# Performance work log

Measured on AMD Instinct MI355X. Metric: run time of the kernel, lower is better.

Reference implementation:

```python
import jax, jax.numpy as jnp
import numpy as np

# geomloss SamplesLoss('sinkhorn', p=2, blur=0.05, scaling=0.5, debias=True) math
P = 2
BLUR = 0.05
SCALING = 0.5
DIAMETER = 64.0  # static conservative bound on point-cloud diameter for randn D=64 data


def _eps_schedule():
    eps_list = []
    e = DIAMETER ** P
    target = BLUR ** P
    while e > target:
        eps_list.append(e)
        e *= SCALING ** P
    eps_list.append(target)
    return np.array(eps_list, dtype=np.float32)


def _cost(x, y):
    # C_ij = ||x_i - y_j||^2 / 2   (p=2 cost of geomloss)
    sq = (jnp.sum(x * x, -1)[:, :, None] * 0.5
          + jnp.sum(y * y, -1)[:, None, :] * 0.5
          - jnp.einsum('bnd,bmd->bnm', x, y))
    return jnp.maximum(sq, 0.0)


def _softmin(eps, C, h):
    # f_i = -eps * log sum_j exp(h_j - C_ij / eps);  C: (B,N,M), h: (B,M)
    return -eps * jax.nn.logsumexp(h[:, None, :] - C / eps, axis=-1)


def setup_inputs() -> dict:
    key = jax.random.key(0)
    k1, k2, k3, k4 = jax.random.split(key, 4)
    B, N, M, D = 8, 2048, 2048, 64
    x = jax.random.normal(k1, (B, N, D), dtype=jnp.float32)
    y = jax.random.normal(k2, (B, M, D), dtype=jnp.float32)
    w1 = jax.random.uniform(k3, (B, N), dtype=jnp.float32) + 0.01
    w2 = jax.random.uniform(k4, (B, M), dtype=jnp.float32) + 0.01
    w1 = w1 / jnp.sum(w1, axis=-1, keepdims=True)
    w2 = w2 / jnp.sum(w2, axis=-1, keepdims=True)
    return {'x': x, 'y': y, 'w1': w1, 'w2': w2}


def _sinkhorn_divergence(x, y, w1, w2):
    a_log = jnp.log(w1)
    b_log = jnp.log(w2)
    eps_list = jnp.asarray(_eps_schedule())

    # --- Sinkhorn loop on detached quantities (geomloss detaches the loop) ---
    xd = jax.lax.stop_gradient(x)
    yd = jax.lax.stop_gradient(y)
    ald = jax.lax.stop_gradient(a_log)
    bld = jax.lax.stop_gradient(b_log)
    C_xy_d = _cost(xd, yd)
    C_yx_d = jnp.swapaxes(C_xy_d, 1, 2)
    C_xx_d = _cost(xd, xd)
    C_yy_d = _cost(yd, yd)

    eps0 = eps_list[0]
    f_ab = _softmin(eps0, C_xy_d, bld)
    g_ba = _softmin(eps0, C_yx_d, ald)
    f_aa = _softmin(eps0, C_xx_d, ald)
    g_bb = _softmin(eps0, C_yy_d, bld)

    def step(carry, eps):
        f_ab, g_ba, f_aa, g_bb = carry
        ft = _softmin(eps, C_xy_d, bld + g_ba / eps)
        gt = _softmin(eps, C_yx_d, ald + f_ab / eps)
        f_aa_t = _softmin(eps, C_xx_d, ald + f_aa / eps)
        g_bb_t = _softmin(eps, C_yy_d, bld + g_bb / eps)
        return (0.5 * (f_ab + ft), 0.5 * (g_ba + gt),
                0.5 * (f_aa + f_aa_t), 0.5 * (g_bb + g_bb_t)), None

    (f_ab, g_ba, f_aa, g_bb), _ = jax.lax.scan(step, (f_ab, g_ba, f_aa, g_bb), eps_list)

    # --- last extrapolation at eps = blur^p, differentiable ---
    eps = eps_list[-1]
    C_xy = _cost(x, y)
    C_yx = jnp.swapaxes(C_xy, 1, 2)
    C_xx = _cost(x, x)
    C_yy = _cost(y, y)
    f_ab_f = _softmin(eps, C_xy, b_log + g_ba / eps)
    g_ba_f = _softmin(eps, C_yx, a_log + f_ab / eps)
    f_aa_f = _softmin(eps, C_xx, a_log + f_aa / eps)
    g_bb_f = _softmin(eps, C_yy, b_log + g_bb / eps)

    # debiased sinkhorn cost per batch element
    loss = (jnp.sum(w1 * (f_ab_f - f_aa_f), axis=-1)
            + jnp.sum(w2 * (g_ba_f - g_bb_f), axis=-1))
    return loss


def reference(x, y, w1, w2):
    loss = _sinkhorn_divergence(x, y, w1, w2)
    return jnp.mean(loss)  # reduction='mean'
```

## Files before the change

kernel.cpp:

```cpp
#include <hip/hip_runtime.h>

#define NB 8
#define NN 2048
#define MM 2048
#define DD 64
#define NCHK 16
#define TS 128
#define L2E 1.4426950408889634f
#define LN2 0.6931471805599453f

typedef _Float16 half_t;
typedef __attribute__((ext_vector_type(8))) _Float16 f16x8;
typedef __attribute__((ext_vector_type(4))) float f32x4;

__device__ half_t g_xh[NB * NN * DD];
__device__ half_t g_yh[NB * MM * DD];
__device__ float g_fab[3][NB * NN], g_gba[3][NB * NN];
__device__ float g_faa[3][NB * NN], g_gbb[3][NB * NN];
__device__ float g_alog[NB * NN], g_blog[NB * NN];
__device__ float g_xn[NB * NN], g_yn[NB * NN];
__device__ float g_h0[NB * MM], g_h1[NB * NN], g_h2[NB * NN], g_h3[NB * MM];
__device__ float2 g_pfab[NB * NCHK * NN];
__device__ float2 g_pgba[NB * NCHK * NN];
__device__ float2 g_pfaa[NB * NCHK * NN];
__device__ float2 g_pgbb[NB * NCHK * NN];

__global__ __launch_bounds__(256) void prep_kernel(
    const float* __restrict__ x, const float* __restrict__ y,
    const float* __restrict__ w1, const float* __restrict__ w2)
{
  int gid = blockIdx.x * 256 + threadIdx.x;
  if (gid < NB * NN) {
    g_alog[gid] = log2f(w1[gid]);
    g_blog[gid] = log2f(w2[gid]);
  }
  int lane = threadIdx.x & 63;
  int row = blockIdx.x * 4 + (threadIdx.x >> 6);
  float xv = x[(size_t)row * DD + lane];
  float yv = y[(size_t)row * DD + lane];
  g_xh[(size_t)row * DD + lane] = (half_t)xv;
  g_yh[(size_t)row * DD + lane] = (half_t)yv;
  float sx = xv * xv;
  float sy = yv * yv;
#pragma unroll
  for (int off = 32; off > 0; off >>= 1) {
    sx += __shfl_down(sx, off);
    sy += __shfl_down(sy, off);
  }
  if (lane == 0) {
    g_xn[row] = 0.5f * sx;
    g_yn[row] = 0.5f * sy;
  }
}

__global__ __launch_bounds__(256) void hprep_kernel(
    const float* __restrict__ fab_in, const float* __restrict__ gba_in,
    const float* __restrict__ faa_in, const float* __restrict__ gbb_in,
    float gs2)
{
  int i = blockIdx.x * 256 + threadIdx.x;
  g_h0[i] = fmaf(gs2, gba_in[i], g_blog[i]);
  g_h1[i] = fmaf(gs2, fab_in[i], g_alog[i]);
  g_h2[i] = fmaf(gs2, faa_in[i], g_alog[i]);
  g_h3[i] = fmaf(gs2, gbb_in[i], g_blog[i]);
}

struct FusedArgs {
  const half_t* Af;
  const half_t* Bf;
  const float* nrow;
  const float* ncol;
  const float* hrow;
  const float* hcol;
  float2* prow;
  float2* pcol;
  int sym;
};

union SharedU {
  half_t stage[2][TS * DD];
  struct {
    float redR[TS][17], redC[TS][17];
    float rowM[TS], colM[TS];
  } r;
};

__global__ __launch_bounds__(256) void tile_fused(
    FusedArgs T0, FusedArgs T1, FusedArgs T2, float keps)
{
  int u = blockIdx.x;
  int slab, b, I, J;
  if (u < 2048) {
    slab = 0; b = u >> 8;
    int tt = u & 255; I = tt >> 4; J = tt & 15;
  } else {
    int v = u - 2048;
    slab = 1 + v / 1088;
    int w2 = v % 1088;
    b = w2 / 136;
    int rem = w2 % 136, ii = 0;
    while (rem >= NCHK - ii) { rem -= NCHK - ii; ++ii; }
    I = ii; J = ii + rem;
  }
  FusedArgs A = (slab == 0) ? T0 : (slab == 1) ? T1 : T2;

  const int t = threadIdx.x;
  const int w = t >> 6, lane = t & 63;
  const int m = lane & 15, quad = lane >> 4;
  const int i0 = I * TS, j0 = J * TS;

  __shared__ SharedU sh;
  char* lb = (char*)&sh;

  {
    const char* gA = (const char*)(A.Af + ((size_t)b * NN + i0) * DD);
    const char* gB = (const char*)(A.Bf + ((size_t)b * MM + j0) * DD);
#pragma unroll
    for (int k = 0; k < 8; ++k) {
      int seg = w * 8 + k;
      int p = (seg * 1024 + lane * 16) & 16383;
      int row = p >> 7, colb = p & 127;
      int colx = colb ^ ((row & 7) << 4);
      const char* src = (seg < 16 ? gA : gB) + (size_t)row * 128 + colx;
      __builtin_amdgcn_global_load_lds(
          (const __attribute__((address_space(1))) unsigned int*)src,
          (__attribute__((address_space(3))) unsigned int*)(lb + seg * 1024),
          16, 0, 0);
    }
  }

  float4 xr[2], hq[2];
#pragma unroll
  for (int g = 0; g < 2; ++g) {
    size_t ro = (size_t)b * NN + i0 + 32 * w + 16 * g + 4 * quad;
    xr[g] = *(const float4*)(A.nrow + ro);
    hq[g] = *(const float4*)(A.hcol + ro);
  }
  float ynk[8], hr[8];
#pragma unroll
  for (int c = 0; c < 8; ++c) {
    size_t co = (size_t)b * MM + j0 + 16 * c + m;
    ynk[c] = -A.ncol[co] * keps;
    hr[c] = A.hrow[co];
  }
  float xnk[2][4], hcv[2][4];
#pragma unroll
  for (int g = 0; g < 2; ++g) {
    xnk[g][0] = -xr[g].x * keps; xnk[g][1] = -xr[g].y * keps;
    xnk[g][2] = -xr[g].z * keps; xnk[g][3] = -xr[g].w * keps;
    hcv[g][0] = hq[g].x; hcv[g][1] = hq[g].y;
    hcv[g][2] = hq[g].z; hcv[g][3] = hq[g].w;
  }

  __syncthreads();

  f32x4 acc[2][8];
#pragma unroll
  for (int g = 0; g < 2; ++g)
#pragma unroll
    for (int c = 0; c < 8; ++c) acc[g][c] = (f32x4){0.f, 0.f, 0.f, 0.f};

#pragma unroll
  for (int s = 0; s < 2; ++s) {
    int qb = quad * 16 + s * 64;
    int ra0 = 32 * w + m, ra1 = 32 * w + 16 + m;
    f16x8 a0 = *(const f16x8*)(lb + ra0 * 128 + (qb ^ ((ra0 & 7) << 4)));
    f16x8 a1 = *(const f16x8*)(lb + ra1 * 128 + (qb ^ ((ra1 & 7) << 4)));
#pragma unroll
    for (int c = 0; c < 8; ++c) {
      int rb = 16 * c + m;
      f16x8 bf = *(const f16x8*)(lb + 16384 + rb * 128 + (qb ^ ((rb & 7) << 4)));
      acc[0][c] = __builtin_amdgcn_mfma_f32_16x16x32_f16(a0, bf, acc[0][c], 0, 0, 0);
      acc[1][c] = __builtin_amdgcn_mfma_f32_16x16x32_f16(a1, bf, acc[1][c], 0, 0, 0);
    }
  }

  float rm[2][4], cm[8];
#pragma unroll
  for (int g = 0; g < 2; ++g)
#pragma unroll
    for (int r = 0; r < 4; ++r) rm[g][r] = -3.0e38f;
#pragma unroll
  for (int c = 0; c < 8; ++c) cm[c] = -3.0e38f;

#pragma unroll
  for (int g = 0; g < 2; ++g)
#pragma unroll
    for (int c = 0; c < 8; ++c) {
      f32x4 v = acc[g][c];
#pragma unroll
      for (int r = 0; r < 4; ++r) {
        float bse = fminf(fmaf(v[r], keps, xnk[g][r]) + ynk[c], 0.f);
        v[r] = bse;
        rm[g][r] = fmaxf(rm[g][r], bse + hr[c]);
        cm[c] = fmaxf(cm[c], bse + hcv[g][r]);
      }
      acc[g][c] = v;
    }

  __syncthreads();

#pragma unroll
  for (int g = 0; g < 2; ++g)
#pragma unroll
    for (int r = 0; r < 4; ++r)
      sh.r.redR[32 * w + 16 * g + 4 * quad + r][m] = rm[g][r];
#pragma unroll
  for (int c = 0; c < 8; ++c)
    sh.r.redC[16 * c + m][4 * w + quad] = cm[c];
  __syncthreads();
  if (t < TS) {
    float mx = sh.r.redR[t][0];
#pragma unroll
    for (int k = 1; k < 16; ++k) mx = fmaxf(mx, sh.r.redR[t][k]);
    sh.r.rowM[t] = mx;
  } else {
    int tt = t - TS;
    float mx = sh.r.redC[tt][0];
#pragma unroll
    for (int k = 1; k < 16; ++k) mx = fmaxf(mx, sh.r.redC[tt][k]);
    sh.r.colM[tt] = mx;
  }
  __syncthreads();

  float rmv[2][4], cmv[8];
#pragma unroll
  for (int g = 0; g < 2; ++g) {
    float4 q = *(const float4*)&sh.r.rowM[32 * w + 16 * g + 4 * quad];
    rmv[g][0] = q.x; rmv[g][1] = q.y; rmv[g][2] = q.z; rmv[g][3] = q.w;
  }
#pragma unroll
  for (int c = 0; c < 8; ++c) cmv[c] = sh.r.colM[16 * c + m];

  float rs[2][4], cs[8];
#pragma unroll
  for (int g = 0; g < 2; ++g)
#pragma unroll
    for (int r = 0; r < 4; ++r) rs[g][r] = 0.f;
#pragma unroll
  for (int c = 0; c < 8; ++c) cs[c] = 0.f;

#pragma unroll
  for (int g = 0; g < 2; ++g)
#pragma unroll
    for (int c = 0; c < 8; ++c) {
      f32x4 v = acc[g][c];
#pragma unroll
      for (int r = 0; r < 4; ++r) {
        rs[g][r] += __builtin_amdgcn_exp2f(v[r] + hr[c] - rmv[g][r]);
        cs[c] += __builtin_amdgcn_exp2f(v[r] + hcv[g][r] - cmv[c]);
      }
    }

#pragma unroll
  for (int g = 0; g < 2; ++g)
#pragma unroll
    for (int r = 0; r < 4; ++r)
      sh.r.redR[32 * w + 16 * g + 4 * quad + r][m] = rs[g][r];
#pragma unroll
  for (int c = 0; c < 8; ++c)
    sh.r.redC[16 * c + m][4 * w + quad] = cs[c];
  __syncthreads();
  if (t < TS) {
    float s = 0.f;
#pragma unroll
    for (int k = 0; k < 16; ++k) s += sh.r.redR[t][k];
    A.prow[((size_t)b * NCHK + J) * NN + i0 + t] = make_float2(sh.r.rowM[t], s);
  } else {
    int tt = t - TS;
    if (!(A.sym && I == J)) {
      float s = 0.f;
#pragma unroll
      for (int k = 0; k < 16; ++k) s += sh.r.redC[tt][k];
      A.pcol[((size_t)b * NCHK + I) * NN + j0 + tt] = make_float2(sh.r.colM[tt], s);
    }
  }
}

struct MergeArgs {
  const float2* part;
  const float* fold;
  float* fout;
  const float* hbase;
  float* hout;
};

__global__ __launch_bounds__(256) void merge4(
    MergeArgs M0, MergeArgs M1, MergeArgs M2, MergeArgs M3,
    float eps, float alpha, float beta, float nextgs)
{
  MergeArgs A = (blockIdx.z == 0) ? M0 : (blockIdx.z == 1) ? M1
              : (blockIdx.z == 2) ? M2 : M3;
  const int b = blockIdx.y;
  const int i = blockIdx.x * 256 + threadIdx.x;
  float2 p[NCHK];
#pragma unroll
  for (int k = 0; k < NCHK; ++k)
    p[k] = A.part[((size_t)b * NCHK + k) * NN + i];
  float M = p[0].x;
#pragma unroll
  for (int k = 1; k < NCHK; ++k) M = fmaxf(M, p[k].x);
  float S = 0.f;
#pragma unroll
  for (int k = 0; k < NCHK; ++k) S += p[k].y * __builtin_amdgcn_exp2f(p[k].x - M);
  float ft = (-LN2 * eps) * (M + __log2f(S));
  int idx = b * NN + i;
  float fnew = alpha * A.fold[idx] + beta * ft;
  A.fout[idx] = fnew;
  A.hout[idx] = fmaf(nextgs * L2E, fnew, A.hbase[idx]);
}

__global__ __launch_bounds__(256) void loss_kernel(
    const float* __restrict__ w1, const float* __restrict__ w2,
    float* __restrict__ out)
{
  __shared__ float red[256];
  float acc = 0.f;
  for (int idx = threadIdx.x; idx < NB * NN; idx += 256) {
    acc += w1[idx] * (g_fab[2][idx] - g_faa[2][idx])
         + w2[idx] * (g_gba[2][idx] - g_gbb[2][idx]);
  }
  red[threadIdx.x] = acc;
  __syncthreads();
  for (int s = 128; s > 0; s >>= 1) {
    if (threadIdx.x < s) red[threadIdx.x] += red[threadIdx.x + s];
    __syncthreads();
  }
  if (threadIdx.x == 0) out[0] = red[0] * (1.0f / NB);
}

extern "C" void kernel_launch(void* const* d_in, const int* in_sizes, int n_in,
                              void* d_out, int out_size, void* d_ws, size_t ws_size,
                              hipStream_t stream)
{
  const float* x = (const float*)d_in[0];
  const float* y = (const float*)d_in[1];
  const float* w1 = (const float*)d_in[2];
  const float* w2 = (const float*)d_in[3];
  float* out = (float*)d_out;

  half_t *xh, *yh;
  float *xn, *yn;
  float *h0, *h1, *h2, *h3, *fabp, *gbap, *faap, *gbbp, *alog, *blog;
  float2 *pfab, *pgba, *pfaa, *pgbb;
  hipGetSymbolAddress((void**)&xh, HIP_SYMBOL(g_xh));
  hipGetSymbolAddress((void**)&yh, HIP_SYMBOL(g_yh));
  hipGetSymbolAddress((void**)&xn, HIP_SYMBOL(g_xn));
  hipGetSymbolAddress((void**)&yn, HIP_SYMBOL(g_yn));
  hipGetSymbolAddress((void**)&h0, HIP_SYMBOL(g_h0));
  hipGetSymbolAddress((void**)&h1, HIP_SYMBOL(g_h1));
  hipGetSymbolAddress((void**)&h2, HIP_SYMBOL(g_h2));
  hipGetSymbolAddress((void**)&h3, HIP_SYMBOL(g_h3));
  hipGetSymbolAddress((void**)&fabp, HIP_SYMBOL(g_fab));
  hipGetSymbolAddress((void**)&gbap, HIP_SYMBOL(g_gba));
  hipGetSymbolAddress((void**)&faap, HIP_SYMBOL(g_faa));
  hipGetSymbolAddress((void**)&gbbp, HIP_SYMBOL(g_gbb));
  hipGetSymbolAddress((void**)&alog, HIP_SYMBOL(g_alog));
  hipGetSymbolAddress((void**)&blog, HIP_SYMBOL(g_blog));
  hipGetSymbolAddress((void**)&pfab, HIP_SYMBOL(g_pfab));
  hipGetSymbolAddress((void**)&pgba, HIP_SYMBOL(g_pgba));
  hipGetSymbolAddress((void**)&pfaa, HIP_SYMBOL(g_pfaa));
  hipGetSymbolAddress((void**)&pgbb, HIP_SYMBOL(g_pgbb));

  auto fab = [&](int s) { return fabp + (size_t)s * NB * NN; };
  auto gba = [&](int s) { return gbap + (size_t)s * NB * NN; };
  auto faa = [&](int s) { return faap + (size_t)s * NB * NN; };
  auto gbb = [&](int s) { return gbbp + (size_t)s * NB * NN; };

  float eps_list[32];
  int ne = 0;
  {
    double v = 64.0 * 64.0;
    double tgt = 0.05 * 0.05;
    while (v > tgt) { eps_list[ne++] = (float)v; v *= 0.25; }
    eps_list[ne++] = (float)tgt;
  }

  prep_kernel<<<4096, 256, 0, stream>>>(x, y, w1, w2);

  dim3 tg(4224);
  dim3 mg(NN / 256, NB, 4);

  auto launch_iter = [&](float eps, float alpha, float beta, float nextgs,
                         int in, int outsel) {
    float keps = L2E / eps;
    FusedArgs T0 = {xh, yh, xn, yn, h0, h1, pfab, pgba, 0};
    FusedArgs T1 = {xh, xh, xn, xn, h2, h2, pfaa, pfaa, 1};
    FusedArgs T2 = {yh, yh, yn, yn, h3, h3, pgbb, pgbb, 1};
    tile_fused<<<tg, 256, 0, stream>>>(T0, T1, T2, keps);
    MergeArgs M0 = {pfab, fab(in), fab(outsel), alog, h1};
    MergeArgs M1 = {pgba, gba(in), gba(outsel), blog, h0};
    MergeArgs M2 = {pfaa, faa(in), faa(outsel), alog, h2};
    MergeArgs M3 = {pgbb, gbb(in), gbb(outsel), blog, h3};
    merge4<<<mg, 256, 0, stream>>>(M0, M1, M2, M3, eps, alpha, beta, nextgs);
  };

  hprep_kernel<<<64, 256, 0, stream>>>(fab(0), gba(0), faa(0), gbb(0), 0.f);
  launch_iter(eps_list[0], 0.f, 1.f, 1.0f / eps_list[0], 0, 0);

  int cur = 0;
  for (int k = 0; k < ne; ++k) {
    int nxt = 1 - cur;
    float nextgs = 1.0f / ((k < ne - 1) ? eps_list[k + 1] : eps_list[ne - 1]);
    launch_iter(eps_list[k], 0.5f, 0.5f, nextgs, cur, nxt);
    cur = nxt;
  }

  launch_iter(eps_list[ne - 1], 0.f, 1.f, 0.f, cur, 2);

  loss_kernel<<<1, 256, 0, stream>>>(w1, w2, out);
}
```

Baseline: 762.6 us.

## Recompute MFMA tile instead of holding accumulators; use wave shuffles for reductions

The fused tile kernel no longer keeps all 64 accumulator floats live across both passes. It reruns the MFMA products per column block in the sum pass, which lowers register pressure and allows a launch bound of 4 blocks per SM. Row max and sum reductions now use in-wave shuffles. Column reductions go through a small [128][4] shared array instead of the large padded reduction buffers, which cuts shared memory use and the number of barriers. The cost is doubling the MFMA and LDS B-fragment reads, plus extra shuffle instructions.

```diff
diff --git a/kernel.cpp b/kernel.cpp
--- a/kernel.cpp
+++ b/kernel.cpp
@@ -77,15 +77,7 @@
   int sym;
 };
 
-union SharedU {
-  half_t stage[2][TS * DD];
-  struct {
-    float redR[TS][17], redC[TS][17];
-    float rowM[TS], colM[TS];
-  } r;
-};
-
-__global__ __launch_bounds__(256) void tile_fused(
+__global__ __launch_bounds__(256, 4) void tile_fused(
     FusedArgs T0, FusedArgs T1, FusedArgs T2, float keps)
 {
   int u = blockIdx.x;
@@ -109,8 +101,9 @@
   const int m = lane & 15, quad = lane >> 4;
   const int i0 = I * TS, j0 = J * TS;
 
-  __shared__ SharedU sh;
-  char* lb = (char*)&sh;
+  __shared__ __align__(16) char stage[2 * TS * DD * 2];
+  __shared__ __align__(16) float cmaxw[TS][4];
+  __shared__ __align__(16) float csumw[TS][4];
 
   {
     const char* gA = (const char*)(A.Af + ((size_t)b * NN + i0) * DD);
@@ -124,7 +117,7 @@
       const char* src = (seg < 16 ? gA : gB) + (size_t)row * 128 + colx;
       __builtin_amdgcn_global_load_lds(
           (const __attribute__((address_space(1))) unsigned int*)src,
-          (__attribute__((address_space(3))) unsigned int*)(lb + seg * 1024),
+          (__attribute__((address_space(3))) unsigned int*)(stage + seg * 1024),
           16, 0, 0);
     }
   }
@@ -154,126 +147,148 @@
 
   __syncthreads();
 
-  f32x4 acc[2][8];
+  const int qb0 = quad * 16, qb1 = quad * 16 + 64;
+  const int ra0 = 32 * w + m, ra1 = 32 * w + 16 + m;
+  const int sa0 = (ra0 & 7) << 4, sa1 = (ra1 & 7) << 4;
+  f16x8 a00 = *(const f16x8*)(stage + ra0 * 128 + (qb0 ^ sa0));
+  f16x8 a01 = *(const f16x8*)(stage + ra0 * 128 + (qb1 ^ sa0));
+  f16x8 a10 = *(const f16x8*)(stage + ra1 * 128 + (qb0 ^ sa1));
+  f16x8 a11 = *(const f16x8*)(stage + ra1 * 128 + (qb1 ^ sa1));
+
+  float rm[2][4], cm8[8];
 #pragma unroll
   for (int g = 0; g < 2; ++g)
 #pragma unroll
-    for (int c = 0; c < 8; ++c) acc[g][c] = (f32x4){0.f, 0.f, 0.f, 0.f};
-
-#pragma unroll
-  for (int s = 0; s < 2; ++s) {
-    int qb = quad * 16 + s * 64;
-    int ra0 = 32 * w + m, ra1 = 32 * w + 16 + m;
-    f16x8 a0 = *(const f16x8*)(lb + ra0 * 128 + (qb ^ ((ra0 & 7) << 4)));
-    f16x8 a1 = *(const f16x8*)(lb + ra1 * 128 + (qb ^ ((ra1 & 7) << 4)));
-#pragma unroll
-    for (int c = 0; c < 8; ++c) {
-      int rb = 16 * c + m;
-      f16x8 bf = *(const f16x8*)(lb + 16384 + rb * 128 + (qb ^ ((rb & 7) << 4)));
-      acc[0][c] = __builtin_amdgcn_mfma_f32_16x16x32_f16(a0, bf, acc[0][c], 0, 0, 0);
-      acc[1][c] = __builtin_amdgcn_mfma_f32_16x16x32_f16(a1, bf, acc[1][c], 0, 0, 0);
-    }
-  }
-
-  float rm[2][4], cm[8];
-#pragma unroll
-  for (int g = 0; g < 2; ++g)
-#pragma unroll
     for (int r = 0; r < 4; ++r) rm[g][r] = -3.0e38f;
-#pragma unroll
-  for (int c = 0; c < 8; ++c) cm[c] = -3.0e38f;
-
-#pragma unroll
-  for (int g = 0; g < 2; ++g)
-#pragma unroll
-    for (int c = 0; c < 8; ++c) {
-      f32x4 v = acc[g][c];
+
+#pragma unroll
+  for (int c = 0; c < 8; ++c) {
+    const int rb = 16 * c + m, sw = (rb & 7) << 4;
+    const char* bp = stage + 16384 + rb * 128;
+    f16x8 b0 = *(const f16x8*)(bp + (qb0 ^ sw));
+    f16x8 b1 = *(const f16x8*)(bp + (qb1 ^ sw));
+    f32x4 acc0 = {0.f, 0.f, 0.f, 0.f}, acc1 = {0.f, 0.f, 0.f, 0.f};
+    acc0 = __builtin_amdgcn_mfma_f32_16x16x32_f16(a00, b0, acc0, 0, 0, 0);
+    acc0 = __builtin_amdgcn_mfma_f32_16x16x32_f16(a01, b1, acc0, 0, 0, 0);
+    acc1 = __builtin_amdgcn_mfma_f32_16x16x32_f16(a10, b0, acc1, 0, 0, 0);
+    acc1 = __builtin_amdgcn_mfma_f32_16x16x32_f16(a11, b1, acc1, 0, 0, 0);
+    float cmc = -3.0e38f;
+#pragma unroll
+    for (int g = 0; g < 2; ++g) {
+      f32x4 v = g ? acc1 : acc0;
 #pragma unroll
       for (int r = 0; r < 4; ++r) {
         float bse = fminf(fmaf(v[r], keps, xnk[g][r]) + ynk[c], 0.f);
-        v[r] = bse;
         rm[g][r] = fmaxf(rm[g][r], bse + hr[c]);
-        cm[c] = fmaxf(cm[c], bse + hcv[g][r]);
-      }
-      acc[g][c] = v;
-    }
-
-  __syncthreads();
-
-#pragma unroll
-  for (int g = 0; g < 2; ++g)
-#pragma unroll
-    for (int r = 0; r < 4; ++r)
-      sh.r.redR[32 * w + 16 * g + 4 * quad + r][m] = rm[g][r];
-#pragma unroll
-  for (int c = 0; c < 8; ++c)
-    sh.r.redC[16 * c + m][4 * w + quad] = cm[c];
-  __syncthreads();
-  if (t < TS) {
-    float mx = sh.r.redR[t][0];
-#pragma unroll
-    for (int k = 1; k < 16; ++k) mx = fmaxf(mx, sh.r.redR[t][k]);
-    sh.r.rowM[t] = mx;
-  } else {
-    int tt = t - TS;
-    float mx = sh.r.redC[tt][0];
-#pragma unroll
-    for (int k = 1; k < 16; ++k) mx = fmaxf(mx, sh.r.redC[tt][k]);
-    sh.r.colM[tt] = mx;
-  }
-  __syncthreads();
-
-  float rmv[2][4], cmv[8];
-#pragma unroll
-  for (int g = 0; g < 2; ++g) {
-    float4 q = *(const float4*)&sh.r.rowM[32 * w + 16 * g + 4 * quad];
-    rmv[g][0] = q.x; rmv[g][1] = q.y; rmv[g][2] = q.z; rmv[g][3] = q.w;
-  }
-#pragma unroll
-  for (int c = 0; c < 8; ++c) cmv[c] = sh.r.colM[16 * c + m];
-
-  float rs[2][4], cs[8];
-#pragma unroll
-  for (int g = 0; g < 2; ++g)
-#pragma unroll
-    for (int r = 0; r < 4; ++r) rs[g][r] = 0.f;
-#pragma unroll
-  for (int c = 0; c < 8; ++c) cs[c] = 0.f;
-
-#pragma unroll
-  for (int g = 0; g < 2; ++g)
-#pragma unroll
-    for (int c = 0; c < 8; ++c) {
-      f32x4 v = acc[g][c];
-#pragma unroll
-      for (int r = 0; r < 4; ++r) {
-        rs[g][r] += __builtin_amdgcn_exp2f(v[r] + hr[c] - rmv[g][r]);
-        cs[c] += __builtin_amdgcn_exp2f(v[r] + hcv[g][r] - cmv[c]);
+        cmc = fmaxf(cmc, bse + hcv[g][r]);
       }
     }
-
+    cm8[c] = cmc;
+  }
+
+  float rmv[2][4];
 #pragma unroll
   for (int g = 0; g < 2; ++g)
 #pragma unroll
-    for (int r = 0; r < 4; ++r)
-      sh.r.redR[32 * w + 16 * g + 4 * quad + r][m] = rs[g][r];
-#pragma unroll
-  for (int c = 0; c < 8; ++c)
-    sh.r.redC[16 * c + m][4 * w + quad] = cs[c];
+    for (int r = 0; r < 4; ++r) {
+      float v = rm[g][r];
+      v = fmaxf(v, __shfl_xor(v, 1));
+      v = fmaxf(v, __shfl_xor(v, 2));
+      v = fmaxf(v, __shfl_xor(v, 4));
+      v = fmaxf(v, __shfl_xor(v, 8));
+      rmv[g][r] = v;
+    }
+
+#pragma unroll
+  for (int c = 0; c < 8; ++c) {
+    float v = cm8[c];
+    v = fmaxf(v, __shfl_xor(v, 16));
+    v = fmaxf(v, __shfl_xor(v, 32));
+    cm8[c] = v;
+  }
+  if (quad == 0) {
+#pragma unroll
+    for (int c = 0; c < 8; ++c) cmaxw[16 * c + m][w] = cm8[c];
+  }
   __syncthreads();
-  if (t < TS) {
-    float s = 0.f;
-#pragma unroll
-    for (int k = 0; k < 16; ++k) s += sh.r.redR[t][k];
-    A.prow[((size_t)b * NCHK + J) * NN + i0 + t] = make_float2(sh.r.rowM[t], s);
-  } else {
-    int tt = t - TS;
-    if (!(A.sym && I == J)) {
-      float s = 0.f;
-#pragma unroll
-      for (int k = 0; k < 16; ++k) s += sh.r.redC[tt][k];
-      A.pcol[((size_t)b * NCHK + I) * NN + j0 + tt] = make_float2(sh.r.colM[tt], s);
+  float cmv[8];
+#pragma unroll
+  for (int c = 0; c < 8; ++c) {
+    float4 q4 = *(const float4*)cmaxw[16 * c + m];
+    cmv[c] = fmaxf(fmaxf(q4.x, q4.y), fmaxf(q4.z, q4.w));
+  }
+
+  float rs[2][4], cs8[8];
+#pragma unroll
+  for (int g = 0; g < 2; ++g)
+#pragma unroll
+    for (int r = 0; r < 4; ++r) rs[g][r] = 0.f;
+
+#pragma unroll
+  for (int c = 0; c < 8; ++c) {
+    const int rb = 16 * c + m, sw = (rb & 7) << 4;
+    const char* bp = stage + 16384 + rb * 128;
+    f16x8 b0 = *(const f16x8*)(bp + (qb0 ^ sw));
+    f16x8 b1 = *(const f16x8*)(bp + (qb1 ^ sw));
+    f32x4 acc0 = {0.f, 0.f, 0.f, 0.f}, acc1 = {0.f, 0.f, 0.f, 0.f};
+    acc0 = __builtin_amdgcn_mfma_f32_16x16x32_f16(a00, b0, acc0, 0, 0, 0);
+    acc0 = __builtin_amdgcn_mfma_f32_16x16x32_f16(a01, b1, acc0, 0, 0, 0);
+    acc1 = __builtin_amdgcn_mfma_f32_16x16x32_f16(a10, b0, acc1, 0, 0, 0);
+    acc1 = __builtin_amdgcn_mfma_f32_16x16x32_f16(a11, b1, acc1, 0, 0, 0);
+    float csc = 0.f;
+#pragma unroll
+    for (int g = 0; g < 2; ++g) {
+      f32x4 v = g ? acc1 : acc0;
+#pragma unroll
+      for (int r = 0; r < 4; ++r) {
+        float bse = fminf(fmaf(v[r], keps, xnk[g][r]) + ynk[c], 0.f);
+        rs[g][r] += __builtin_amdgcn_exp2f(bse + hr[c] - rmv[g][r]);
+        csc += __builtin_amdgcn_exp2f(bse + hcv[g][r] - cmv[c]);
+      }
     }
+    cs8[c] = csc;
+  }
+
+#pragma unroll
+  for (int g = 0; g < 2; ++g)
+#pragma unroll
+    for (int r = 0; r < 4; ++r) {
+      float v = rs[g][r];
+      v += __shfl_xor(v, 1);
+      v += __shfl_xor(v, 2);
+      v += __shfl_xor(v, 4);
+      v += __shfl_xor(v, 8);
+      rs[g][r] = v;
+    }
+  if (m == 0) {
+    float2* pr = A.prow + ((size_t)b * NCHK + J) * NN + i0;
+#pragma unroll
+    for (int g = 0; g < 2; ++g)
+#pragma unroll
+      for (int r = 0; r < 4; ++r) {
+        int row = 32 * w + 16 * g + 4 * quad + r;
+        pr[row] = make_float2(rmv[g][r], rs[g][r]);
+      }
+  }
+
+#pragma unroll
+  for (int c = 0; c < 8; ++c) {
+    float v = cs8[c];
+    v += __shfl_xor(v, 16);
+    v += __shfl_xor(v, 32);
+    cs8[c] = v;
+  }
+  if (quad == 0) {
+#pragma unroll
+    for (int c = 0; c < 8; ++c) csumw[16 * c + m][w] = cs8[c];
+  }
+  __syncthreads();
+  if (t < TS && !(A.sym && I == J)) {
+    float4 mq = *(const float4*)cmaxw[t];
+    float4 sq = *(const float4*)csumw[t];
+    float M = fmaxf(fmaxf(mq.x, mq.y), fmaxf(mq.z, mq.w));
+    float S = sq.x + sq.y + sq.z + sq.w;
+    A.pcol[((size_t)b * NCHK + I) * NN + j0 + t] = make_float2(M, S);
   }
 }
 
```

Result: slower. 1.095 ms (+43.5%).

## Split 128x128 tile across 8 waves and use packed float2 epilogue math

Applied to the files above, without the earlier changes.

The fused tile kernel now runs with 512 threads (8 waves), so each wave handles 16 rows instead of 32. This halves per-thread accumulators and loads, and changes the shared-memory reduction layout to 32 partials per column. The epilogue is rewritten with 2-wide float vectors so the compiler can emit packed FP32 ops. The aim is lower register pressure and more latency hiding. The cost is more waves reducing through LDS, an extra reduction width, and a larger block.

```diff
diff --git a/kernel.cpp b/kernel.cpp
--- a/kernel.cpp
+++ b/kernel.cpp
@@ -12,6 +12,10 @@
 typedef _Float16 half_t;
 typedef __attribute__((ext_vector_type(8))) _Float16 f16x8;
 typedef __attribute__((ext_vector_type(4))) float f32x4;
+typedef __attribute__((ext_vector_type(2))) float f32x2;
+
+__device__ inline f32x2 lo2(f32x4 v) { return __builtin_shufflevector(v, v, 0, 1); }
+__device__ inline f32x2 hi2(f32x4 v) { return __builtin_shufflevector(v, v, 2, 3); }
 
 __device__ half_t g_xh[NB * NN * DD];
 __device__ half_t g_yh[NB * MM * DD];
@@ -77,15 +81,7 @@
   int sym;
 };
 
-union SharedU {
-  half_t stage[2][TS * DD];
-  struct {
-    float redR[TS][17], redC[TS][17];
-    float rowM[TS], colM[TS];
-  } r;
-};
-
-__global__ __launch_bounds__(256) void tile_fused(
+__global__ __launch_bounds__(512) void tile_fused(
     FusedArgs T0, FusedArgs T1, FusedArgs T2, float keps)
 {
   int u = blockIdx.x;
@@ -109,33 +105,32 @@
   const int m = lane & 15, quad = lane >> 4;
   const int i0 = I * TS, j0 = J * TS;
 
-  __shared__ SharedU sh;
-  char* lb = (char*)&sh;
+  __shared__ __align__(16) char sh[32768];
+  float* redR = (float*)sh;
+  float* redC = (float*)(sh + 8704);
+  float* rowM = (float*)(sh + 25600);
+  float* colM = (float*)(sh + 26112);
 
   {
     const char* gA = (const char*)(A.Af + ((size_t)b * NN + i0) * DD);
     const char* gB = (const char*)(A.Bf + ((size_t)b * MM + j0) * DD);
 #pragma unroll
-    for (int k = 0; k < 8; ++k) {
-      int seg = w * 8 + k;
+    for (int k = 0; k < 4; ++k) {
+      int seg = w * 4 + k;
       int p = (seg * 1024 + lane * 16) & 16383;
       int row = p >> 7, colb = p & 127;
       int colx = colb ^ ((row & 7) << 4);
       const char* src = (seg < 16 ? gA : gB) + (size_t)row * 128 + colx;
       __builtin_amdgcn_global_load_lds(
           (const __attribute__((address_space(1))) unsigned int*)src,
-          (__attribute__((address_space(3))) unsigned int*)(lb + seg * 1024),
+          (__attribute__((address_space(3))) unsigned int*)(sh + seg * 1024),
           16, 0, 0);
     }
   }
 
-  float4 xr[2], hq[2];
-#pragma unroll
-  for (int g = 0; g < 2; ++g) {
-    size_t ro = (size_t)b * NN + i0 + 32 * w + 16 * g + 4 * quad;
-    xr[g] = *(const float4*)(A.nrow + ro);
-    hq[g] = *(const float4*)(A.hcol + ro);
-  }
+  size_t ro = (size_t)b * NN + i0 + 16 * w + 4 * quad;
+  float4 xr = *(const float4*)(A.nrow + ro);
+  float4 hq = *(const float4*)(A.hcol + ro);
   float ynk[8], hr[8];
 #pragma unroll
   for (int c = 0; c < 8; ++c) {
@@ -143,136 +138,126 @@
     ynk[c] = -A.ncol[co] * keps;
     hr[c] = A.hrow[co];
   }
-  float xnk[2][4], hcv[2][4];
-#pragma unroll
-  for (int g = 0; g < 2; ++g) {
-    xnk[g][0] = -xr[g].x * keps; xnk[g][1] = -xr[g].y * keps;
-    xnk[g][2] = -xr[g].z * keps; xnk[g][3] = -xr[g].w * keps;
-    hcv[g][0] = hq[g].x; hcv[g][1] = hq[g].y;
-    hcv[g][2] = hq[g].z; hcv[g][3] = hq[g].w;
-  }
-
-  __syncthreads();
-
-  f32x4 acc[2][8];
-#pragma unroll
-  for (int g = 0; g < 2; ++g)
-#pragma unroll
-    for (int c = 0; c < 8; ++c) acc[g][c] = (f32x4){0.f, 0.f, 0.f, 0.f};
-
-#pragma unroll
-  for (int s = 0; s < 2; ++s) {
-    int qb = quad * 16 + s * 64;
-    int ra0 = 32 * w + m, ra1 = 32 * w + 16 + m;
-    f16x8 a0 = *(const f16x8*)(lb + ra0 * 128 + (qb ^ ((ra0 & 7) << 4)));
-    f16x8 a1 = *(const f16x8*)(lb + ra1 * 128 + (qb ^ ((ra1 & 7) << 4)));
-#pragma unroll
-    for (int c = 0; c < 8; ++c) {
-      int rb = 16 * c + m;
-      f16x8 bf = *(const f16x8*)(lb + 16384 + rb * 128 + (qb ^ ((rb & 7) << 4)));
-      acc[0][c] = __builtin_amdgcn_mfma_f32_16x16x32_f16(a0, bf, acc[0][c], 0, 0, 0);
-      acc[1][c] = __builtin_amdgcn_mfma_f32_16x16x32_f16(a1, bf, acc[1][c], 0, 0, 0);
-    }
-  }
-
-  float rm[2][4], cm[8];
-#pragma unroll
-  for (int g = 0; g < 2; ++g)
-#pragma unroll
-    for (int r = 0; r < 4; ++r) rm[g][r] = -3.0e38f;
-#pragma unroll
-  for (int c = 0; c < 8; ++c) cm[c] = -3.0e38f;
-
-#pragma unroll
-  for (int g = 0; g < 2; ++g)
-#pragma unroll
-    for (int c = 0; c < 8; ++c) {
-      f32x4 v = acc[g][c];
-#pragma unroll
-      for (int r = 0; r < 4; ++r) {
-        float bse = fminf(fmaf(v[r], keps, xnk[g][r]) + ynk[c], 0.f);
-        v[r] = bse;
-        rm[g][r] = fmaxf(rm[g][r], bse + hr[c]);
-        cm[c] = fmaxf(cm[c], bse + hcv[g][r]);
-      }
-      acc[g][c] = v;
-    }
-
-  __syncthreads();
-
-#pragma unroll
-  for (int g = 0; g < 2; ++g)
-#pragma unroll
-    for (int r = 0; r < 4; ++r)
-      sh.r.redR[32 * w + 16 * g + 4 * quad + r][m] = rm[g][r];
-#pragma unroll
-  for (int c = 0; c < 8; ++c)
-    sh.r.redC[16 * c + m][4 * w + quad] = cm[c];
-  __syncthreads();
-  if (t < TS) {
-    float mx = sh.r.redR[t][0];
-#pragma unroll
-    for (int k = 1; k < 16; ++k) mx = fmaxf(mx, sh.r.redR[t][k]);
-    sh.r.rowM[t] = mx;
-  } else {
-    int tt = t - TS;
-    float mx = sh.r.redC[tt][0];
-#pragma unroll
-    for (int k = 1; k < 16; ++k) mx = fmaxf(mx, sh.r.redC[tt][k]);
-    sh.r.colM[tt] = mx;
-  }
-  __syncthreads();
-
-  float rmv[2][4], cmv[8];
-#pragma unroll
-  for (int g = 0; g < 2; ++g) {
-    float4 q = *(const float4*)&sh.r.rowM[32 * w + 16 * g + 4 * quad];
-    rmv[g][0] = q.x; rmv[g][1] = q.y; rmv[g][2] = q.z; rmv[g][3] = q.w;
-  }
-#pragma unroll
-  for (int c = 0; c < 8; ++c) cmv[c] = sh.r.colM[16 * c + m];
-
-  float rs[2][4], cs[8];
-#pragma unroll
-  for (int g = 0; g < 2; ++g)
-#pragma unroll
-    for (int r = 0; r < 4; ++r) rs[g][r] = 0.f;
-#pragma unroll
-  for (int c = 0; c < 8; ++c) cs[c] = 0.f;
-
-#pragma unroll
-  for (int g = 0; g < 2; ++g)
-#pragma unroll
-    for (int c = 0; c < 8; ++c) {
-      f32x4 v = acc[g][c];
-#pragma unroll
-      for (int r = 0; r < 4; ++r) {
-        rs[g][r] += __builtin_amdgcn_exp2f(v[r] + hr[c] - rmv[g][r]);
-        cs[c] += __builtin_amdgcn_exp2f(v[r] + hcv[g][r] - cmv[c]);
-      }
-    }
-
-#pragma unroll
-  for (int g = 0; g < 2; ++g)
-#pragma unroll
-    for (int r = 0; r < 4; ++r)
-      sh.r.redR[32 * w + 16 * g + 4 * quad + r][m] = rs[g][r];
-#pragma unroll
-  for (int c = 0; c < 8; ++c)
-    sh.r.redC[16 * c + m][4 * w + quad] = cs[c];
-  __syncthreads();
-  if (t < TS) {
+  f32x2 xnkp0 = {-xr.x * keps, -xr.y * keps};
+  f32x2 xnkp1 = {-xr.z * keps, -xr.w * keps};
+  f32x2 hcp0 = {hq.x, hq.y}, hcp1 = {hq.z, hq.w};
+
+  __syncthreads();
+
+  const int qb0 = quad * 16, qb1 = qb0 + 64;
+  const int ra = 16 * w + m, sa = (ra & 7) << 4;
+  f16x8 a0 = *(const f16x8*)(sh + ra * 128 + (qb0 ^ sa));
+  f16x8 a1 = *(const f16x8*)(sh + ra * 128 + (qb1 ^ sa));
+
+  const int sb = (m & 7) << 4;
+  const char* bb = sh + 16384 + m * 128;
+  f32x4 acc[8];
+#pragma unroll
+  for (int c = 0; c < 8; ++c) {
+    f16x8 b0 = *(const f16x8*)(bb + c * 2048 + (qb0 ^ sb));
+    f16x8 b1 = *(const f16x8*)(bb + c * 2048 + (qb1 ^ sb));
+    f32x4 a = {0.f, 0.f, 0.f, 0.f};
+    a = __builtin_amdgcn_mfma_f32_16x16x32_f16(a0, b0, a, 0, 0, 0);
+    a = __builtin_amdgcn_mfma_f32_16x16x32_f16(a1, b1, a, 0, 0, 0);
+    acc[c] = a;
+  }
+
+  const f32x2 kv = {keps, keps};
+  const f32x2 zz = {0.f, 0.f};
+  f32x2 rmp0 = {-3.0e38f, -3.0e38f}, rmp1 = {-3.0e38f, -3.0e38f};
+  float cm[8];
+#pragma unroll
+  for (int c = 0; c < 8; ++c) {
+    f32x2 ay0 = xnkp0 + ynk[c];
+    f32x2 ay1 = xnkp1 + ynk[c];
+    f32x2 q0 = __builtin_elementwise_fma(lo2(acc[c]), kv, ay0);
+    f32x2 q1 = __builtin_elementwise_fma(hi2(acc[c]), kv, ay1);
+    f32x2 b0 = __builtin_elementwise_min(q0, zz);
+    f32x2 b1 = __builtin_elementwise_min(q1, zz);
+    acc[c] = __builtin_shufflevector(b0, b1, 0, 1, 2, 3);
+    f32x2 rv0 = b0 + hr[c];
+    f32x2 rv1 = b1 + hr[c];
+    rmp0 = __builtin_elementwise_max(rmp0, rv0);
+    rmp1 = __builtin_elementwise_max(rmp1, rv1);
+    f32x2 cv0 = b0 + hcp0;
+    f32x2 cv1 = b1 + hcp1;
+    cm[c] = fmaxf(fmaxf(cv0.x, cv0.y), fmaxf(cv1.x, cv1.y));
+  }
+
+  __syncthreads();
+
+  {
+    int rbase = (16 * w + 4 * quad) * 17 + m;
+    redR[rbase] = rmp0.x; redR[rbase + 17] = rmp0.y;
+    redR[rbase + 34] = rmp1.x; redR[rbase + 51] = rmp1.y;
+    int cidx = m * 33 + 4 * w + quad;
+#pragma unroll
+    for (int c = 0; c < 8; ++c) redC[cidx + c * 528] = cm[c];
+  }
+  __syncthreads();
+
+  if (t < 128) {
+    float mx = redR[t * 17];
+#pragma unroll
+    for (int k = 1; k < 16; ++k) mx = fmaxf(mx, redR[t * 17 + k]);
+    rowM[t] = mx;
+  } else if (t < 256) {
+    int cc = t - 128;
+    float mx = redC[cc * 33];
+#pragma unroll
+    for (int k = 1; k < 32; ++k) mx = fmaxf(mx, redC[cc * 33 + k]);
+    colM[cc] = mx;
+  }
+  __syncthreads();
+
+  float4 rq = *(const float4*)(rowM + 16 * w + 4 * quad);
+  f32x2 rmv0 = {rq.x, rq.y}, rmv1 = {rq.z, rq.w};
+  float cmv[8];
+#pragma unroll
+  for (int c = 0; c < 8; ++c) cmv[c] = colM[16 * c + m];
+
+  f32x2 rsp0 = {0.f, 0.f}, rsp1 = {0.f, 0.f};
+  float cs[8];
+#pragma unroll
+  for (int c = 0; c < 8; ++c) {
+    f32x2 hrm0 = hr[c] - rmv0;
+    f32x2 hrm1 = hr[c] - rmv1;
+    f32x2 chm0 = hcp0 - cmv[c];
+    f32x2 chm1 = hcp1 - cmv[c];
+    f32x2 b0 = lo2(acc[c]), b1 = hi2(acc[c]);
+    f32x2 t0 = b0 + hrm0, t1 = b1 + hrm1;
+    float e0 = __builtin_amdgcn_exp2f(t0.x), e1 = __builtin_amdgcn_exp2f(t0.y);
+    float e2 = __builtin_amdgcn_exp2f(t1.x), e3 = __builtin_amdgcn_exp2f(t1.y);
+    f32x2 ep0 = {e0, e1}, ep1 = {e2, e3};
+    rsp0 += ep0; rsp1 += ep1;
+    f32x2 u0 = b0 + chm0, u1 = b1 + chm1;
+    float f0 = __builtin_amdgcn_exp2f(u0.x), f1 = __builtin_amdgcn_exp2f(u0.y);
+    float f2 = __builtin_amdgcn_exp2f(u1.x), f3 = __builtin_amdgcn_exp2f(u1.y);
+    cs[c] = (f0 + f1) + (f2 + f3);
+  }
+
+  {
+    int rbase = (16 * w + 4 * quad) * 17 + m;
+    redR[rbase] = rsp0.x; redR[rbase + 17] = rsp0.y;
+    redR[rbase + 34] = rsp1.x; redR[rbase + 51] = rsp1.y;
+    int cidx = m * 33 + 4 * w + quad;
+#pragma unroll
+    for (int c = 0; c < 8; ++c) redC[cidx + c * 528] = cs[c];
+  }
+  __syncthreads();
+
+  if (t < 128) {
     float s = 0.f;
 #pragma unroll
-    for (int k = 0; k < 16; ++k) s += sh.r.redR[t][k];
-    A.prow[((size_t)b * NCHK + J) * NN + i0 + t] = make_float2(sh.r.rowM[t], s);
-  } else {
-    int tt = t - TS;
+    for (int k = 0; k < 16; ++k) s += redR[t * 17 + k];
+    A.prow[((size_t)b * NCHK + J) * NN + i0 + t] = make_float2(rowM[t], s);
+  } else if (t < 256) {
     if (!(A.sym && I == J)) {
+      int cc = t - 128;
       float s = 0.f;
 #pragma unroll
-      for (int k = 0; k < 16; ++k) s += sh.r.redC[tt][k];
-      A.pcol[((size_t)b * NCHK + I) * NN + j0 + tt] = make_float2(sh.r.colM[tt], s);
+      for (int k = 0; k < 32; ++k) s += redC[cc * 33 + k];
+      A.pcol[((size_t)b * NCHK + I) * NN + j0 + cc] = make_float2(colM[cc], s);
     }
   }
 }
@@ -387,7 +372,7 @@
     FusedArgs T0 = {xh, yh, xn, yn, h0, h1, pfab, pgba, 0};
     FusedArgs T1 = {xh, xh, xn, xn, h2, h2, pfaa, pfaa, 1};
     FusedArgs T2 = {yh, yh, yn, yn, h3, h3, pgbb, pgbb, 1};
-    tile_fused<<<tg, 256, 0, stream>>>(T0, T1, T2, keps);
+    tile_fused<<<tg, 512, 0, stream>>>(T0, T1, T2, keps);
     MergeArgs M0 = {pfab, fab(in), fab(outsel), alog, h1};
     MergeArgs M1 = {pgba, gba(in), gba(outsel), blog, h0};
     MergeArgs M2 = {pfaa, faa(in), faa(outsel), alog, h2};
```

Result: faster. 712.9 us (-6.5%).
